# Kernel optimization log

Measured on AMD Instinct MI355X. Metric: run time of the kernel, lower is better.

The kernel has to match this reference:

```python
import jax, jax.numpy as jnp
import numpy as np

HIDDEN = 32          # config.model_hidden_channels
KSIZE = 3            # dilated conv kernel size
DIL = 3              # dilated conv dilation
SLOPE = 0.2          # leaky relu slope

B, L = 16, 32768
HOP = 256
KL = L // HOP        # kernel_length = 128
LVC_K = 3            # location-variable conv kernel size
OUT = 2 * HIDDEN     # gated output channels


def _leaky(x):
    return jnp.where(x >= 0, x, SLOPE * x)


def setup_inputs() -> dict:
    key = jax.random.key(0)
    k1, k2, k3, k4, k5 = jax.random.split(key, 5)
    return {
        "hidden_states": jax.random.normal(k1, (B, HIDDEN, L), dtype=jnp.float32),
        "kernel": jax.random.normal(k2, (B, HIDDEN, OUT, LVC_K, KL), dtype=jnp.float32) * 0.1,
        "bias": jax.random.normal(k3, (B, OUT, KL), dtype=jnp.float32) * 0.1,
        "conv_w": jax.random.normal(k4, (HIDDEN, HIDDEN, KSIZE), dtype=jnp.float32) * (1.0 / np.sqrt(HIDDEN * KSIZE)),
        "conv_b": jax.random.normal(k5, (HIDDEN,), dtype=jnp.float32) * 0.01,
        "hop_size": HOP,
    }


def reference(hidden_states, kernel, bias, conv_w, conv_b, hop_size):
    residual = hidden_states
    x = _leaky(hidden_states)
    # dilated Conv1d, 'same' padding
    pad = DIL * (KSIZE - 1) // 2
    x = jax.lax.conv_general_dilated(
        x, conv_w, window_strides=(1,), padding=[(pad, pad)],
        rhs_dilation=(DIL,), dimension_numbers=("NCH", "OIH", "NCH"))
    x = x + conv_b[None, :, None]
    x = _leaky(x)

    # location-variable convolution (dilation=1 path of the torch code)
    b, c, in_len = x.shape
    _, _, out_ch, k, kl = kernel.shape
    p = (k - 1) // 2
    xp = jnp.pad(x, ((0, 0), (0, 0), (p, p)))           # (B, C, L+2p)
    # sliding windows of size k at every position (equivalent of the unfolds)
    idx = jnp.arange(in_len)[:, None] + jnp.arange(k)[None, :]   # (L, k)
    win = xp[:, :, idx]                                  # (B, C, L, k)
    win = win.reshape(b, c, kl, hop_size, k)             # (B, C, KL, hop, k)
    # per-segment local GEMM: einsum 'bildsk,biokl->bolsd' with d==1
    out = jnp.einsum("bilsk,biokl->bols", win, kernel)   # (B, O, KL, hop)
    out = out + bias[:, :, :, None]
    out = out.reshape(b, out_ch, in_len)                 # (B, 2C, L)

    # gated activation + residual
    y = jax.nn.sigmoid(out[:, :HIDDEN, :]) * jnp.tanh(out[:, HIDDEN:, :])
    return residual + y
```

## Files before the change

### kernel.cpp

```cpp
#include <hip/hip_runtime.h>

static constexpr int HID = 32;
static constexpr int LEN = 32768;
static constexpr int NKL = 128;
static constexpr int HOP = 256;
#define SLOPE 0.2f

typedef short short8 __attribute__((ext_vector_type(8)));
typedef float floatx4 __attribute__((ext_vector_type(4)));
typedef unsigned int u32;

static constexpr int XROW  = 64;
static constexpr int WOFF  = 17792;
static constexpr int WROW  = 208;
static constexpr int WSLAB = 64 * WROW;
static constexpr int SMEMB = WOFF + WSLAB;

__device__ __forceinline__ int xsw(int row, int bcol) {
    return ((row << 6) + bcol) ^ ((row & 7) << 4);
}

static constexpr size_t KT_USH  = (size_t)16 * NKL * 64 * 104;
static constexpr size_t CWT_OFF = KT_USH;

__device__ __forceinline__ float leaky(float x) { return fmaxf(x, SLOPE * x); }

__device__ __forceinline__ unsigned short f2bf(float f) {
    union { float f; unsigned u; } v; v.f = f;
    unsigned r = v.u + 0x7FFFu + ((v.u >> 16) & 1u);
    return (unsigned short)(r >> 16);
}
__device__ __forceinline__ u32 cvtpk(float lo, float hi) {
    u32 r;
    asm("v_cvt_pk_bf16_f32 %0, %1, %2" : "=v"(r) : "v"(lo), "v"(hi));
    return r;
}
__device__ __forceinline__ float rcp_fast(float x) {
    float r; asm("v_rcp_f32 %0, %1" : "=v"(r) : "v"(x)); return r;
}
__device__ __forceinline__ float gatef(float a, float c) {
    float sg = rcp_fast(1.0f + __expf(-a));
    float t  = fmaf(-2.0f, rcp_fast(1.0f + __expf(2.0f * c)), 1.0f);
    return sg * t;
}

__global__ __launch_bounds__(256) void prep_kern(
    const float* __restrict__ kern,
    const float* __restrict__ cw,
    unsigned short* __restrict__ kt)
{
    const int blk = blockIdx.x;
    const int b = blk >> 6, o = blk & 63;
    const int tid = threadIdx.x;
    __shared__ unsigned short lt[32 * 386];

    const float* src = kern + (size_t)(b * 2048 + o) * 384;
    #pragma unroll
    for (int j = 0; j < 12; ++j) {
        const int f = tid + 256 * j;
        const int i = f / 96, r = f - i * 96;
        float4 v = *(const float4*)(src + (size_t)i * 24576 + (size_t)r * 4);
        *(u32*)(lt + i * 386 + r * 4)     = cvtpk(v.x, v.y);
        *(u32*)(lt + i * 386 + r * 4 + 2) = cvtpk(v.z, v.w);
    }

    if (blk == 0) {
        #pragma unroll
        for (int j = 0; j < 12; ++j) {
            const int d = tid + 256 * j;
            const int o2 = d / 96, rr = d - o2 * 96;
            const int kk = rr >> 5, i = rr & 31;
            kt[CWT_OFF + d] = f2bf(cw[(o2 * 32 + i) * 3 + kk]);
        }
    }
    __syncthreads();

    unsigned short* slab = kt + (size_t)b * (NKL * 64 * 104) + (size_t)o * 104;
    #pragma unroll
    for (int j = 0; j < 7; ++j) {
        const int s = tid + 256 * j;
        if (s < 1664) {
            const int kl = s / 13, q = s - kl * 13;
            uint4 d = make_uint4(0u, 0u, 0u, 0u);
            if (q < 12) {
                const int kk = q >> 2;
                const int ib = 8 * (q & 3);
                const unsigned short* p = lt + kk * 128 + kl;
                d.x = (u32)p[(ib + 0) * 386] | ((u32)p[(ib + 1) * 386] << 16);
                d.y = (u32)p[(ib + 2) * 386] | ((u32)p[(ib + 3) * 386] << 16);
                d.z = (u32)p[(ib + 4) * 386] | ((u32)p[(ib + 5) * 386] << 16);
                d.w = (u32)p[(ib + 6) * 386] | ((u32)p[(ib + 7) * 386] << 16);
            }
            *(uint4*)(slab + (size_t)kl * 6656 + 8 * q) = d;
        }
    }
}

__global__ __launch_bounds__(256, 5) void univnet_mfma(
    const float* __restrict__ h,
    const float* __restrict__ bias,
    const float* __restrict__ cb,
    float* __restrict__ out,
    const unsigned short* __restrict__ kt)
{
    __shared__ __align__(16) char smem[SMEMB];

    const int blk = blockIdx.x;
    const int b   = blk & 15;
    const int kl  = blk >> 4;
    const int t0  = kl * HOP;
    const int p0  = t0 - 4;
    const int tid = threadIdx.x;
    const int w   = tid >> 6;
    const int lane = tid & 63;
    const int l15 = lane & 15;
    const int l4  = lane >> 4;

    const float* hb = h + (size_t)b * (HID * LEN);
    const bool edge = (kl == 0) || (kl == NKL - 1);

    {
        const char* slab = (const char*)kt + (size_t)(b * NKL + kl) * WSLAB;
        #pragma unroll
        for (int j = 0; j < 4; ++j) {
            const int c = w + 4 * j;
            if (c < 13)
                __builtin_amdgcn_global_load_lds(
                    (const u32 __attribute__((address_space(1)))*)(slab + c * 1024 + lane * 16),
                    (u32 __attribute__((address_space(3)))*)(smem + WOFF + c * 1024),
                    16, 0, 0);
        }
    }

    const unsigned short* cwt = kt + CWT_OFF;
    short8 b1f[2][3];
    #pragma unroll
    for (int tn = 0; tn < 2; ++tn)
        #pragma unroll
        for (int qk = 0; qk < 3; ++qk)
            b1f[tn][qk] = *(const short8*)(cwt + (tn * 16 + l15) * 96 + qk * 32 + l4 * 8);
    float4 cbq[2];
    cbq[0] = *(const float4*)(cb + l4 * 4);
    cbq[1] = *(const float4*)(cb + 16 + l4 * 4);
    float bv[2][2];
    #pragma unroll
    for (int pp = 0; pp < 2; ++pp) {
        bv[pp][0] = bias[((size_t)b * 64 + pp * 16 + l15) * NKL + kl];
        bv[pp][1] = bias[((size_t)b * 64 + pp * 16 + l15 + 32) * NKL + kl];
    }

    {
        auto stage = [&](int tau) {
            const int oct = tau & 3, cq = tau >> 2;
            u32 pk[4][4];
            if (!edge) {
                #pragma unroll
                for (int jp = 0; jp < 4; ++jp) {
                    const int i0 = oct * 8 + 2 * jp;
                    float4 f0 = *(const float4*)(hb + (size_t)i0 * LEN + p0 + 4 * cq);
                    float4 f1 = *(const float4*)(hb + (size_t)(i0 + 1) * LEN + p0 + 4 * cq);
                    pk[0][jp] = cvtpk(leaky(f0.x), leaky(f1.x));
                    pk[1][jp] = cvtpk(leaky(f0.y), leaky(f1.y));
                    pk[2][jp] = cvtpk(leaky(f0.z), leaky(f1.z));
                    pk[3][jp] = cvtpk(leaky(f0.w), leaky(f1.w));
                }
            } else {
                #pragma unroll
                for (int jp = 0; jp < 4; ++jp) {
                    const int i0 = oct * 8 + 2 * jp;
                    #pragma unroll
                    for (int e = 0; e < 4; ++e) {
                        const int p = p0 + 4 * cq + e;
                        float a = 0.0f, c2 = 0.0f;
                        if ((unsigned)p < (unsigned)LEN) {
                            a  = hb[(size_t)i0 * LEN + p];
                            c2 = hb[(size_t)(i0 + 1) * LEN + p];
                        }
                        pk[e][jp] = cvtpk(leaky(a), leaky(c2));
                    }
                }
            }
            #pragma unroll
            for (int e = 0; e < 4; ++e)
                *(uint4*)(smem + xsw(4 * cq + e, oct * 16)) =
                    make_uint4(pk[e][0], pk[e][1], pk[e][2], pk[e][3]);
        };
        stage(tid);
        if (tid < 8) stage(256 + tid);
        if (tid < 224) ((u32*)(smem + 16896))[tid] = 0u;
    }

    __syncthreads();

    floatx4 cacc[9];
    #pragma unroll
    for (int n = 0; n < 9; ++n) {
        const int tt = w + 4 * n;
        if (tt < 34) {
            const int tm = tt >> 1, tn = tt & 1;
            short8 af[3];
            #pragma unroll
            for (int qk = 0; qk < 3; ++qk)
                af[qk] = *(const short8*)(smem + xsw(tm * 16 + l15 + 3 * qk, l4 * 16));
            floatx4 acc = {cbq[tn].x, cbq[tn].y, cbq[tn].z, cbq[tn].w};
            #pragma unroll
            for (int qk = 0; qk < 3; ++qk)
                acc = __builtin_amdgcn_mfma_f32_16x16x32_bf16(b1f[tn][qk], af[qk], acc, 0, 0, 0);
            cacc[n] = acc;
        }
    }
    __syncthreads();

    #pragma unroll
    for (int n = 0; n < 9; ++n) {
        const int tt = w + 4 * n;
        if (tt < 34) {
            const int tm = tt >> 1, tn = tt & 1;
            const int c_out = tm * 16 + l15;
            const int p = t0 - 1 + c_out;
            u32 q0 = 0u, q1 = 0u;
            if ((unsigned)p < (unsigned)LEN) {
                q0 = cvtpk(leaky(cacc[n][0]), leaky(cacc[n][1]));
                q1 = cvtpk(leaky(cacc[n][2]), leaky(cacc[n][3]));
            }
            *(uint2*)(smem + xsw(c_out, tn * 32 + l4 * 8)) = make_uint2(q0, q1);
        }
    }
    __syncthreads();

    #pragma unroll
    for (int pp = 0; pp < 2; ++pp) {
        const int oA = pp * 16 + l15, oB = oA + 32;
        const float* hrow = hb + (size_t)oA * LEN + t0 + w * 16 + l4 * 4;
        const float4 h0 = *(const float4*)(hrow);
        const float4 h1 = *(const float4*)(hrow + 64);
        const float4 h2 = *(const float4*)(hrow + 128);
        const float4 h3 = *(const float4*)(hrow + 192);
        short8 b2A[3], b2B[3];
        #pragma unroll
        for (int qk = 0; qk < 3; ++qk) {
            b2A[qk] = *(const short8*)(smem + WOFF + oA * WROW + (qk * 32 + l4 * 8) * 2);
            b2B[qk] = *(const short8*)(smem + WOFF + oB * WROW + (qk * 32 + l4 * 8) * 2);
        }
        const float bA = bv[pp][0], bB = bv[pp][1];
        float* orow = out + ((size_t)b * HID + oA) * LEN + t0 + w * 16 + l4 * 4;
#define LVC_T(T, HV)                                                            \
        {                                                                       \
            const int tm = 4 * (T) + w;                                         \
            short8 af0 = *(const short8*)(smem + xsw(tm * 16 + l15,     l4 * 16)); \
            short8 af1 = *(const short8*)(smem + xsw(tm * 16 + l15 + 1, l4 * 16)); \
            short8 af2 = *(const short8*)(smem + xsw(tm * 16 + l15 + 2, l4 * 16)); \
            floatx4 aA = {bA, bA, bA, bA}, aB = {bB, bB, bB, bB};               \
            aA = __builtin_amdgcn_mfma_f32_16x16x32_bf16(af0, b2A[0], aA, 0, 0, 0); \
            aB = __builtin_amdgcn_mfma_f32_16x16x32_bf16(af0, b2B[0], aB, 0, 0, 0); \
            aA = __builtin_amdgcn_mfma_f32_16x16x32_bf16(af1, b2A[1], aA, 0, 0, 0); \
            aB = __builtin_amdgcn_mfma_f32_16x16x32_bf16(af1, b2B[1], aB, 0, 0, 0); \
            aA = __builtin_amdgcn_mfma_f32_16x16x32_bf16(af2, b2A[2], aA, 0, 0, 0); \
            aB = __builtin_amdgcn_mfma_f32_16x16x32_bf16(af2, b2B[2], aB, 0, 0, 0); \
            float4 ov;                                                          \
            ov.x = HV.x + gatef(aA[0], aB[0]);                                  \
            ov.y = HV.y + gatef(aA[1], aB[1]);                                  \
            ov.z = HV.z + gatef(aA[2], aB[2]);                                  \
            ov.w = HV.w + gatef(aA[3], aB[3]);                                  \
            *(float4*)(orow + (T) * 64) = ov;                                   \
        }
        LVC_T(0, h0)
        LVC_T(1, h1)
        LVC_T(2, h2)
        LVC_T(3, h3)
#undef LVC_T
    }
}

extern "C" void kernel_launch(void* const* d_in, const int* in_sizes, int n_in,
                              void* d_out, int out_size, void* d_ws, size_t ws_size,
                              hipStream_t stream) {
    const float* h    = (const float*)d_in[0];
    const float* kern = (const float*)d_in[1];
    const float* bias = (const float*)d_in[2];
    const float* cw   = (const float*)d_in[3];
    const float* cb   = (const float*)d_in[4];
    float* outp = (float*)d_out;
    unsigned short* kt = (unsigned short*)d_ws;

    prep_kern<<<1024, 256, 0, stream>>>(kern, cw, kt);
    univnet_mfma<<<2048, 256, 0, stream>>>(h, bias, cb, outp, kt);
}
```

Baseline: 216.2 us.

## Load LVC weight fragments directly from global, drop LDS staging and padding

The per-segment LVC weight slab is no longer staged into shared memory with global_load_lds. Each lane now reads its bf16 B-fragments straight from global memory, and the prep kernel writes an unpadded 96-column layout instead of the 104-column padded one. Shared memory per block shrinks, so launch bounds are raised to 8 blocks per CU for higher occupancy. The cost is uncached global loads of the weights sitting on the MFMA critical path, where the old async LDS prefetch had hidden that latency.

```diff
diff --git a/kernel.cpp b/kernel.cpp
--- a/kernel.cpp
+++ b/kernel.cpp
@@ -11,16 +11,15 @@
 typedef unsigned int u32;
 
 static constexpr int XROW  = 64;
-static constexpr int WOFF  = 17792;
-static constexpr int WROW  = 208;
-static constexpr int WSLAB = 64 * WROW;
-static constexpr int SMEMB = WOFF + WSLAB;
+static constexpr int SMEMB = 17792;
 
 __device__ __forceinline__ int xsw(int row, int bcol) {
     return ((row << 6) + bcol) ^ ((row & 7) << 4);
 }
 
-static constexpr size_t KT_USH  = (size_t)16 * NKL * 64 * 104;
+static constexpr int    B2COLS  = 96;
+static constexpr int    B2SLAB  = 64 * B2COLS;
+static constexpr size_t KT_USH  = (size_t)16 * NKL * 64 * B2COLS;
 static constexpr size_t CWT_OFF = KT_USH;
 
 __device__ __forceinline__ float leaky(float x) { return fmaxf(x, SLOPE * x); }
@@ -75,28 +74,24 @@
     }
     __syncthreads();
 
-    unsigned short* slab = kt + (size_t)b * (NKL * 64 * 104) + (size_t)o * 104;
-    #pragma unroll
-    for (int j = 0; j < 7; ++j) {
+    unsigned short* slab = kt + (size_t)b * (NKL * 64 * B2COLS) + (size_t)o * B2COLS;
+    #pragma unroll
+    for (int j = 0; j < 6; ++j) {
         const int s = tid + 256 * j;
-        if (s < 1664) {
-            const int kl = s / 13, q = s - kl * 13;
-            uint4 d = make_uint4(0u, 0u, 0u, 0u);
-            if (q < 12) {
-                const int kk = q >> 2;
-                const int ib = 8 * (q & 3);
-                const unsigned short* p = lt + kk * 128 + kl;
-                d.x = (u32)p[(ib + 0) * 386] | ((u32)p[(ib + 1) * 386] << 16);
-                d.y = (u32)p[(ib + 2) * 386] | ((u32)p[(ib + 3) * 386] << 16);
-                d.z = (u32)p[(ib + 4) * 386] | ((u32)p[(ib + 5) * 386] << 16);
-                d.w = (u32)p[(ib + 6) * 386] | ((u32)p[(ib + 7) * 386] << 16);
-            }
-            *(uint4*)(slab + (size_t)kl * 6656 + 8 * q) = d;
-        }
-    }
-}
-
-__global__ __launch_bounds__(256, 5) void univnet_mfma(
+        const int kl = s / 12, q = s - kl * 12;
+        const int kk = q >> 2;
+        const int ib = 8 * (q & 3);
+        const unsigned short* p = lt + kk * 128 + kl;
+        uint4 d;
+        d.x = (u32)p[(ib + 0) * 386] | ((u32)p[(ib + 1) * 386] << 16);
+        d.y = (u32)p[(ib + 2) * 386] | ((u32)p[(ib + 3) * 386] << 16);
+        d.z = (u32)p[(ib + 4) * 386] | ((u32)p[(ib + 5) * 386] << 16);
+        d.w = (u32)p[(ib + 6) * 386] | ((u32)p[(ib + 7) * 386] << 16);
+        *(uint4*)(slab + (size_t)kl * B2SLAB + 8 * q) = d;
+    }
+}
+
+__global__ __launch_bounds__(256, 8) void univnet_mfma(
     const float* __restrict__ h,
     const float* __restrict__ bias,
     const float* __restrict__ cb,
@@ -118,19 +113,6 @@
 
     const float* hb = h + (size_t)b * (HID * LEN);
     const bool edge = (kl == 0) || (kl == NKL - 1);
-
-    {
-        const char* slab = (const char*)kt + (size_t)(b * NKL + kl) * WSLAB;
-        #pragma unroll
-        for (int j = 0; j < 4; ++j) {
-            const int c = w + 4 * j;
-            if (c < 13)
-                __builtin_amdgcn_global_load_lds(
-                    (const u32 __attribute__((address_space(1)))*)(slab + c * 1024 + lane * 16),
-                    (u32 __attribute__((address_space(3)))*)(smem + WOFF + c * 1024),
-                    16, 0, 0);
-        }
-    }
 
     const unsigned short* cwt = kt + CWT_OFF;
     short8 b1f[2][3];
@@ -228,6 +210,7 @@
     }
     __syncthreads();
 
+    const unsigned short* b2s = kt + (size_t)(b * NKL + kl) * B2SLAB;
     #pragma unroll
     for (int pp = 0; pp < 2; ++pp) {
         const int oA = pp * 16 + l15, oB = oA + 32;
@@ -236,12 +219,14 @@
         const float4 h1 = *(const float4*)(hrow + 64);
         const float4 h2 = *(const float4*)(hrow + 128);
         const float4 h3 = *(const float4*)(hrow + 192);
-        short8 b2A[3], b2B[3];
-        #pragma unroll
-        for (int qk = 0; qk < 3; ++qk) {
-            b2A[qk] = *(const short8*)(smem + WOFF + oA * WROW + (qk * 32 + l4 * 8) * 2);
-            b2B[qk] = *(const short8*)(smem + WOFF + oB * WROW + (qk * 32 + l4 * 8) * 2);
-        }
+        const unsigned short* rA = b2s + oA * B2COLS + l4 * 8;
+        const unsigned short* rB = b2s + oB * B2COLS + l4 * 8;
+        const short8 b2A0 = *(const short8*)(rA);
+        const short8 b2A1 = *(const short8*)(rA + 32);
+        const short8 b2A2 = *(const short8*)(rA + 64);
+        const short8 b2B0 = *(const short8*)(rB);
+        const short8 b2B1 = *(const short8*)(rB + 32);
+        const short8 b2B2 = *(const short8*)(rB + 64);
         const float bA = bv[pp][0], bB = bv[pp][1];
         float* orow = out + ((size_t)b * HID + oA) * LEN + t0 + w * 16 + l4 * 4;
 #define LVC_T(T, HV)                                                            \
@@ -251,12 +236,12 @@
             short8 af1 = *(const short8*)(smem + xsw(tm * 16 + l15 + 1, l4 * 16)); \
             short8 af2 = *(const short8*)(smem + xsw(tm * 16 + l15 + 2, l4 * 16)); \
             floatx4 aA = {bA, bA, bA, bA}, aB = {bB, bB, bB, bB};               \
-            aA = __builtin_amdgcn_mfma_f32_16x16x32_bf16(af0, b2A[0], aA, 0, 0, 0); \
-            aB = __builtin_amdgcn_mfma_f32_16x16x32_bf16(af0, b2B[0], aB, 0, 0, 0); \
-            aA = __builtin_amdgcn_mfma_f32_16x16x32_bf16(af1, b2A[1], aA, 0, 0, 0); \
-            aB = __builtin_amdgcn_mfma_f32_16x16x32_bf16(af1, b2B[1], aB, 0, 0, 0); \
-            aA = __builtin_amdgcn_mfma_f32_16x16x32_bf16(af2, b2A[2], aA, 0, 0, 0); \
-            aB = __builtin_amdgcn_mfma_f32_16x16x32_bf16(af2, b2B[2], aB, 0, 0, 0); \
+            aA = __builtin_amdgcn_mfma_f32_16x16x32_bf16(af0, b2A0, aA, 0, 0, 0); \
+            aB = __builtin_amdgcn_mfma_f32_16x16x32_bf16(af0, b2B0, aB, 0, 0, 0); \
+            aA = __builtin_amdgcn_mfma_f32_16x16x32_bf16(af1, b2A1, aA, 0, 0, 0); \
+            aB = __builtin_amdgcn_mfma_f32_16x16x32_bf16(af1, b2B1, aB, 0, 0, 0); \
+            aA = __builtin_amdgcn_mfma_f32_16x16x32_bf16(af2, b2A2, aA, 0, 0, 0); \
+            aB = __builtin_amdgcn_mfma_f32_16x16x32_bf16(af2, b2B2, aB, 0, 0, 0); \
             float4 ov;                                                          \
             ov.x = HV.x + gatef(aA[0], aB[0]);                                  \
             ov.y = HV.y + gatef(aA[1], aB[1]);                                  \
```

Measured after the change: 282.8 us. 1.31x slower.
